# Performance work log

Hardware: AMD Instinct MI355X
Metric: run time of the kernel (lower is better)

Reference implementation:

```python
import jax, jax.numpy as jnp
import numpy as np

N, E, G = 100000, 400000, 2000
D = 128            # dim_node
DE = 128 + 300     # dim_edge after RBF concat
NC = 300           # RBF centers
CUT_LO, CUT_HI = 0.0, 30.0
N_CONV = 3


def setup_inputs() -> dict:
    key = jax.random.key(0)
    ks = jax.random.split(key, 32)
    inp = {}
    inp['Z'] = jax.random.randint(ks[0], (N,), 0, 20)
    inp['edge_type'] = jax.random.randint(ks[1], (E,), 0, 400)
    inp['dist'] = jax.random.uniform(ks[2], (E,), dtype=jnp.float32) * CUT_HI
    inp['src'] = jax.random.randint(ks[3], (E,), 0, N)
    inp['dst'] = jax.random.randint(ks[4], (E,), 0, N)
    inp['graph_ids'] = jnp.sort(jax.random.randint(ks[5], (N,), 0, G))
    s = 0.05
    inp['node_emb'] = jax.random.normal(ks[6], (20, D), jnp.float32) * s
    inp['edge_emb'] = jax.random.normal(ks[7], (400, D), jnp.float32) * s
    # per-conv-layer weights, stacked over layer dim
    inp['Wn1'] = jax.random.normal(ks[8], (N_CONV, D, D), jnp.float32) * s
    inp['bn1'] = jnp.zeros((N_CONV, D), jnp.float32)
    inp['Wn2'] = jax.random.normal(ks[9], (N_CONV, D, D), jnp.float32) * s
    inp['bn2'] = jnp.zeros((N_CONV, D), jnp.float32)
    inp['We1'] = jax.random.normal(ks[10], (N_CONV, DE, DE), jnp.float32) * s
    inp['be1'] = jnp.zeros((N_CONV, DE), jnp.float32)
    inp['We2'] = jax.random.normal(ks[11], (N_CONV, D, DE), jnp.float32) * s
    inp['be2'] = jnp.zeros((N_CONV, D), jnp.float32)
    inp['Wc'] = jax.random.normal(ks[12], (N_CONV, D, D), jnp.float32) * s
    inp['bc'] = jnp.zeros((N_CONV, D), jnp.float32)
    # read layer
    inp['Wr1'] = jax.random.normal(ks[13], (D, D), jnp.float32) * s
    inp['br1'] = jnp.zeros((D,), jnp.float32)
    inp['Wr2'] = jax.random.normal(ks[14], (1, D), jnp.float32) * s
    inp['br2'] = jnp.zeros((1,), jnp.float32)
    return inp


def _rbf(dist):
    centers = jnp.linspace(CUT_LO, CUT_HI, NC, dtype=jnp.float32)
    gap = centers[1] - centers[0]
    # [E, NC]
    return jnp.exp(-((dist[:, None] - centers[None, :]) ** 2) / gap)


def reference(Z, edge_type, dist, src, dst, graph_ids,
              node_emb, edge_emb,
              Wn1, bn1, Wn2, bn2, We1, be1, We2, be2, Wc, bc,
              Wr1, br1, Wr2, br2):
    h = node_emb[Z]                          # [N, D] node embedding
    e = edge_emb[edge_type]                  # [E, D] edge embedding
    e = jnp.concatenate([e, _rbf(dist)], axis=1)   # [E, DE]
    for i in range(N_CONV):
        hs = h[src]                          # gather src node feats [E, D]
        hn = jax.nn.relu(hs @ Wn1[i].T + bn1[i]) @ Wn2[i].T + bn2[i]   # [E, D]
        ee = jax.nn.relu(e @ We1[i].T + be1[i]) @ We2[i].T + be2[i]    # [E, D]
        m = jnp.tanh((hn * ee) @ Wc[i].T + bc[i])                      # [E, D]
        h = h + jax.ops.segment_sum(m, dst, num_segments=N)            # scatter-sum
    r = jax.nn.relu(h @ Wr1.T + br1) @ Wr2.T + br2                     # [N, 1]
    out = jax.ops.segment_sum(r, graph_ids, num_segments=G)            # [G, 1]
    return out.flatten()                                               # [G]
```

## Files before the change

kernel.cpp:

```cpp
#include <hip/hip_runtime.h>

#define NN 100000
#define En 400000
#define Gn 2000
#define GRID 2048

typedef unsigned short u16;
typedef unsigned int u32;
typedef _Float16 f16;
typedef f16 f16x8 __attribute__((ext_vector_type(8)));
typedef float f32x4 __attribute__((ext_vector_type(4)));

__device__ __forceinline__ void lds_barrier() {
  asm volatile("s_waitcnt lgkmcnt(0)\ns_barrier" ::: "memory");
}

#define MFMA16(a, b, c) __builtin_amdgcn_mfma_f32_16x16x32_f16(a, b, c, 0, 0, 0)


__global__ __launch_bounds__(256) void k_prepw(
    const float* __restrict__ Wn1, const float* __restrict__ Wn2,
    const float* __restrict__ Wc, const float* __restrict__ We2,
    const float* __restrict__ We1,
    f16* __restrict__ Wn1b, f16* __restrict__ Wn2b, f16* __restrict__ Wcb,
    f16* __restrict__ We2b, f16* __restrict__ Rb) {
  int i = blockIdx.x * 256 + threadIdx.x;
  if (i < 49152) {
    Wn1b[i] = (f16)Wn1[i];
  } else if (i < 98304) {
    int j = i - 49152;
    Wn2b[j] = (f16)Wn2[j];
  } else if (i < 147456) {
    int j = i - 98304;
    Wcb[j] = (f16)Wc[j];
  } else if (i < 319488) {
    int j = i - 147456;
    int l = j / 57344;
    int r = j - l * 57344;
    int row = r / 448;
    int k = r - row * 448;
    float v = (k < 428) ? We2[l * 54784 + row * 428 + k] : 0.f;
    We2b[j] = (f16)v;
  } else if (i < 749568) {
    int j = i - 319488;
    int l = j / 143360;
    int r = j - l * 143360;
    int row = r / 320;
    int k = r - row * 320;
    float v = 0.f;
    if (row < 428 && k < 300) v = We1[(size_t)l * 183184 + row * 428 + 128 + k];
    Rb[j] = (f16)v;
  }
}


__global__ __launch_bounds__(256) void k_t2(const float* __restrict__ edge_emb,
                                            const float* __restrict__ We1,
                                            const float* __restrict__ be1,
                                            f16* __restrict__ T2) {
  __shared__ __align__(16) float sWe[64][32 * 4];
  __shared__ float sB[64];
  const int tid = threadIdx.x;
  const int l = blockIdx.x / 28;
  const int rb = blockIdx.x - l * 28;
  const int jb = rb >> 2;
  const int tc = rb & 3;
  const int j0 = jb * 64;
  for (int idx = tid; idx < 64 * 32; idx += 256) {
    int row = idx >> 5, c = idx & 31;
    int gj = j0 + row;
    float4 v = make_float4(0.f, 0.f, 0.f, 0.f);
    if (gj < 428)
      v = *(const float4*)&We1[(size_t)l * 183184 + gj * 428 + c * 4];
    *(float4*)&sWe[row][c * 4] = v;
  }
  if (tid < 64) {
    int gj = j0 + tid;
    sB[tid] = (gj < 428) ? be1[l * 428 + gj] : 0.f;
  }
  lds_barrier();
  const int jl = tid & 63, tl = tid >> 6;
  const int gj = j0 + jl;
  for (int it = 0; it < 25; ++it) {
    int t = tc * 100 + it * 4 + tl;
    const float4* er = (const float4*)(edge_emb + t * 128);
    float s = 0.f;
#pragma unroll
    for (int d = 0; d < 32; ++d) {
      float4 a = er[d];
      float4 b = *(const float4*)&sWe[jl][d * 4];
      s += a.x * b.x + a.y * b.y + a.z * b.z + a.w * b.w;
    }
    s += sB[jl];
    T2[l * 179200 + t * 448 + gj] = (gj < 428) ? (f16)s : (f16)0.f;
  }
}

__global__ __launch_bounds__(256) void k_dtab(const f16* __restrict__ Rb,
                                              f16* __restrict__ Dtab) {
  const int tid = threadIdx.x;
  int l = blockIdx.x / (GRID + 1);
  int g = blockIdx.x - l * (GRID + 1);
  float d = (float)g * (30.f / (float)GRID);
  int kc = (int)(d * (299.f / 30.f) + 0.5f);
  int kk0 = min(max(kc - 16, 0), 268);
  __shared__ float sE[32];
  if (tid < 32) {
    float x = d - (float)(kk0 + tid) * (30.f / 299.f);
    sE[tid] = __expf(-x * x * (299.f / 30.f));
  }
  __syncthreads();
  for (int j = tid; j < 448; j += 256) {
    const f16* rr = &Rb[((size_t)l * 448 + j) * 320 + kk0];
    float s = 0.f;
#pragma unroll
    for (int k = 0; k < 32; ++k) s += sE[k] * (float)rr[k];
    Dtab[((size_t)(l * (GRID + 1) + g)) * 448 + j] = (f16)s;
  }
}


__global__ __launch_bounds__(256) void k_zero32(u32* __restrict__ p, int n) {
  int i = blockIdx.x * 256 + threadIdx.x;
  if (i < n) p[i] = 0u;
}

__global__ __launch_bounds__(256) void k_hist(const int* __restrict__ dstv,
                                              u32* __restrict__ hist) {
  int e = blockIdx.x * 256 + threadIdx.x;
  if (e < En) atomicAdd(&hist[dstv[e]], 1u);
}

__global__ __launch_bounds__(1024) void k_scan1(const u32* __restrict__ hist,
                                                u32* __restrict__ excl,
                                                u32* __restrict__ part) {
  __shared__ u32 s[1024];
  const int t = threadIdx.x, b = blockIdx.x, i = b * 1024 + t;
  u32 v = (i < NN) ? hist[i] : 0u;
  s[t] = v;
  __syncthreads();
  u32 acc = v;
  for (int off = 1; off < 1024; off <<= 1) {
    u32 add = (t >= off) ? s[t - off] : 0u;
    __syncthreads();
    acc += add;
    s[t] = acc;
    __syncthreads();
  }
  if (i < NN) excl[i] = acc - v;
  if (t == 1023) part[b] = acc;
}

__global__ __launch_bounds__(128) void k_scan2(u32* __restrict__ part, int n) {
  __shared__ u32 s[128];
  const int t = threadIdx.x;
  u32 v = (t < n) ? part[t] : 0u;
  s[t] = v;
  __syncthreads();
  u32 acc = v;
  for (int off = 1; off < 128; off <<= 1) {
    u32 add = (t >= off) ? s[t - off] : 0u;
    __syncthreads();
    acc += add;
    s[t] = acc;
    __syncthreads();
  }
  if (t < n) part[t] = acc - v;
}

__global__ __launch_bounds__(1024) void k_scan3(const u32* __restrict__ excl,
                                                const u32* __restrict__ part,
                                                u32* __restrict__ cursor) {
  int i = blockIdx.x * 1024 + threadIdx.x;
  if (i < NN) cursor[i] = excl[i] + part[blockIdx.x];
}

__global__ __launch_bounds__(256) void k_scatter(const int* __restrict__ etype,
                                                 const float* __restrict__ dist,
                                                 const int* __restrict__ srcv,
                                                 const int* __restrict__ dstv,
                                                 u32* __restrict__ cursor,
                                                 int4* __restrict__ epack,
                                                 int* __restrict__ edst) {
  int e = blockIdx.x * 256 + threadIdx.x;
  if (e >= En) return;
  int d = dstv[e];
  int pos = (int)atomicAdd(&cursor[d], 1u);
  float fi = dist[e] * ((float)GRID / 30.f);
  int ix = (int)fi;
  epack[pos] = make_int4(srcv[e], etype[e] * 448, ix * 448,
                         __float_as_int(fi - (float)ix));
  edst[pos] = d;
}


__global__ __launch_bounds__(256) void k_node(const float* __restrict__ h,
                                              const f16* __restrict__ W1,
                                              const float* __restrict__ b1,
                                              const f16* __restrict__ W2,
                                              const float* __restrict__ b2,
                                              f16* __restrict__ n2) {
  __shared__ __align__(16) f16 sH[64 * 136];
  __shared__ __align__(16) f16 sT[64 * 136];
  const int tid = threadIdx.x;
  const int nbase = blockIdx.x * 64;
  for (int i = tid; i < 64 * 128; i += 256) {
    int e = i >> 7, d = i & 127;
    int node = nbase + e;
    float v = (node < NN) ? h[(size_t)node * 128 + d] : 0.f;
    sH[e * 136 + d] = (f16)v;
  }
  lds_barrier();
  const int lane = tid & 63, wave = tid >> 6;
  const int q = lane >> 4, ln = lane & 15;
  const int nb = wave * 32;

  f32x4 acc[4][2];
#pragma unroll
  for (int m = 0; m < 4; ++m)
#pragma unroll
    for (int n = 0; n < 2; ++n) acc[m][n] = 0.f;
#pragma unroll
  for (int k0 = 0; k0 < 128; k0 += 32) {
    f16x8 a[4];
#pragma unroll
    for (int m = 0; m < 4; ++m)
      a[m] = *(const f16x8*)&sH[(m * 16 + ln) * 136 + k0 + q * 8];
#pragma unroll
    for (int n = 0; n < 2; ++n) {
      f16x8 b = *(const f16x8*)&W1[(nb + n * 16 + ln) * 128 + k0 + q * 8];
#pragma unroll
      for (int m = 0; m < 4; ++m) acc[m][n] = MFMA16(a[m], b, acc[m][n]);
    }
  }
#pragma unroll
  for (int n = 0; n < 2; ++n) {
    int col = nb + n * 16 + ln;
    float bb = b1[col];
#pragma unroll
    for (int m = 0; m < 4; ++m)
#pragma unroll
      for (int r = 0; r < 4; ++r) {
        int row = m * 16 + q * 4 + r;
        sT[row * 136 + col] = (f16)fmaxf(acc[m][n][r] + bb, 0.f);
      }
  }
  lds_barrier();

  f32x4 acc2[4][2];
#pragma unroll
  for (int m = 0; m < 4; ++m)
#pragma unroll
    for (int n = 0; n < 2; ++n) acc2[m][n] = 0.f;
#pragma unroll
  for (int k0 = 0; k0 < 128; k0 += 32) {
    f16x8 a[4];
#pragma unroll
    for (int m = 0; m < 4; ++m)
      a[m] = *(const f16x8*)&sT[(m * 16 + ln) * 136 + k0 + q * 8];
#pragma unroll
    for (int n = 0; n < 2; ++n) {
      f16x8 b = *(const f16x8*)&W2[(nb + n * 16 + ln) * 128 + k0 + q * 8];
#pragma unroll
      for (int m = 0; m < 4; ++m) acc2[m][n] = MFMA16(a[m], b, acc2[m][n]);
    }
  }
#pragma unroll
  for (int n = 0; n < 2; ++n) {
    int col = nb + n * 16 + ln;
    float bb = b2[col];
#pragma unroll
    for (int m = 0; m < 4; ++m)
#pragma unroll
      for (int r = 0; r < 4; ++r) {
        int row = m * 16 + q * 4 + r;
        int node = nbase + row;
        if (node < NN) n2[(size_t)node * 128 + col] = (f16)(acc2[m][n][r] + bb);
      }
  }
}


__global__ __launch_bounds__(256) void k_node0(const int* __restrict__ Z,
                                               const float* __restrict__ node_emb,
                                               const f16* __restrict__ W1,
                                               const float* __restrict__ b1,
                                               const f16* __restrict__ W2,
                                               const float* __restrict__ b2,
                                               f16* __restrict__ n2,
                                               float* __restrict__ h,
                                               float* __restrict__ out) {
  __shared__ __align__(16) f16 sH[64 * 136];
  __shared__ __align__(16) f16 sT[64 * 136];
  __shared__ int sZ[64];
  const int tid = threadIdx.x;
  const int nbase = blockIdx.x * 64;
  {
    int oi = blockIdx.x * 256 + tid;
    if (oi < Gn) out[oi] = 0.f;
  }
  if (tid < 64) sZ[tid] = Z[min(nbase + tid, NN - 1)];
  lds_barrier();
  for (int i = tid; i < 64 * 128; i += 256) {
    int e = i >> 7, d = i & 127;
    int node = nbase + e;
    float v = node_emb[sZ[e] * 128 + d];
    sH[e * 136 + d] = (f16)v;
    if (node < NN) h[(size_t)node * 128 + d] = v;
  }
  lds_barrier();
  const int lane = tid & 63, wave = tid >> 6;
  const int q = lane >> 4, ln = lane & 15;
  const int nb = wave * 32;

  f32x4 acc[4][2];
#pragma unroll
  for (int m = 0; m < 4; ++m)
#pragma unroll
    for (int n = 0; n < 2; ++n) acc[m][n] = 0.f;
#pragma unroll
  for (int k0 = 0; k0 < 128; k0 += 32) {
    f16x8 a[4];
#pragma unroll
    for (int m = 0; m < 4; ++m)
      a[m] = *(const f16x8*)&sH[(m * 16 + ln) * 136 + k0 + q * 8];
#pragma unroll
    for (int n = 0; n < 2; ++n) {
      f16x8 b = *(const f16x8*)&W1[(nb + n * 16 + ln) * 128 + k0 + q * 8];
#pragma unroll
      for (int m = 0; m < 4; ++m) acc[m][n] = MFMA16(a[m], b, acc[m][n]);
    }
  }
#pragma unroll
  for (int n = 0; n < 2; ++n) {
    int col = nb + n * 16 + ln;
    float bb = b1[col];
#pragma unroll
    for (int m = 0; m < 4; ++m)
#pragma unroll
      for (int r = 0; r < 4; ++r) {
        int row = m * 16 + q * 4 + r;
        sT[row * 136 + col] = (f16)fmaxf(acc[m][n][r] + bb, 0.f);
      }
  }
  lds_barrier();

  f32x4 acc2[4][2];
#pragma unroll
  for (int m = 0; m < 4; ++m)
#pragma unroll
    for (int n = 0; n < 2; ++n) acc2[m][n] = 0.f;
#pragma unroll
  for (int k0 = 0; k0 < 128; k0 += 32) {
    f16x8 a[4];
#pragma unroll
    for (int m = 0; m < 4; ++m)
      a[m] = *(const f16x8*)&sT[(m * 16 + ln) * 136 + k0 + q * 8];
#pragma unroll
    for (int n = 0; n < 2; ++n) {
      f16x8 b = *(const f16x8*)&W2[(nb + n * 16 + ln) * 128 + k0 + q * 8];
#pragma unroll
      for (int m = 0; m < 4; ++m) acc2[m][n] = MFMA16(a[m], b, acc2[m][n]);
    }
  }
#pragma unroll
  for (int n = 0; n < 2; ++n) {
    int col = nb + n * 16 + ln;
    float bb = b2[col];
#pragma unroll
    for (int m = 0; m < 4; ++m)
#pragma unroll
      for (int r = 0; r < 4; ++r) {
        int row = m * 16 + q * 4 + r;
        int node = nbase + row;
        if (node < NN) n2[(size_t)node * 128 + col] = (f16)(acc2[m][n][r] + bb);
      }
  }
}


__global__ __launch_bounds__(256)
__attribute__((amdgpu_waves_per_eu(4, 4))) void k_edge(
    const int4* __restrict__ epack, const int* __restrict__ edst,
    const f16* __restrict__ T2, const f16* __restrict__ Dtab,
    const f16* __restrict__ We2b, const float* __restrict__ be2,
    const f16* __restrict__ Wcb, const float* __restrict__ bc,
    const f16* __restrict__ n2, float* __restrict__ h) {
  __shared__ __align__(16) f16 sC[2][64 * 136];
  __shared__ int sSrc[64], sDst[64], sT2o[64], sIdx[64];
  __shared__ float sFrac[64];

  const int tid = threadIdx.x;
  const int e0 = blockIdx.x * 64;
  if (tid < 64) {
    int4 p = epack[e0 + tid];
    sSrc[tid] = p.x;
    sT2o[tid] = p.y;
    sIdx[tid] = p.z;
    sFrac[tid] = __int_as_float(p.w);
    sDst[tid] = edst[e0 + tid];
  }
  lds_barrier();

  const int lane = tid & 63, wave = tid >> 6;
  const int q = lane >> 4, ln = lane & 15;
  const int nb = wave * 32;

  f32x4 acc[4][2];
#pragma unroll
  for (int m = 0; m < 4; ++m)
#pragma unroll
    for (int n = 0; n < 2; ++n) acc[m][n] = 0.f;

  auto lerp_relu = [](f16x8 lo, f16x8 hi, f16x8 t2, f16 fr) -> f16x8 {
    f16x8 v = t2 + lo + (hi - lo) * fr;
    f16x8 z = {};
    return __builtin_elementwise_max(v, z);
  };
  auto pf128 = [&](int k0, f16x8* plo, f16x8* phi, f16x8* pt2, f16* pfr) {
    const int cg = tid & 15, eb = tid >> 4;
    const int col = k0 + cg * 8;
#pragma unroll
    for (int i = 0; i < 4; ++i) {
      int e = eb + i * 16;
      int off = sIdx[e] + col;
      plo[i] = *(const f16x8*)&Dtab[off];
      phi[i] = *(const f16x8*)&Dtab[off + 448];
      pt2[i] = *(const f16x8*)&T2[sT2o[e] + col];
      pfr[i] = (f16)sFrac[e];
    }
  };
  auto st128 = [&](f16* buf, const f16x8* plo, const f16x8* phi,
                   const f16x8* pt2, const f16* pfr) {
    const int cg = tid & 15, eb = tid >> 4;
#pragma unroll
    for (int i = 0; i < 4; ++i) {
      int e = eb + i * 16;
      *(f16x8*)&buf[e * 136 + cg * 8] = lerp_relu(plo[i], phi[i], pt2[i], pfr[i]);
    }
  };
  auto pf64 = [&](f16x8* plo, f16x8* phi, f16x8* pt2, f16* pfr) {
    const int cg = tid & 7, eb = tid >> 3;
    const int col = 384 + cg * 8;
#pragma unroll
    for (int i = 0; i < 2; ++i) {
      int e = eb + i * 32;
      int off = sIdx[e] + col;
      plo[i] = *(const f16x8*)&Dtab[off];
      phi[i] = *(const f16x8*)&Dtab[off + 448];
      pt2[i] = *(const f16x8*)&T2[sT2o[e] + col];
      pfr[i] = (f16)sFrac[e];
    }
  };
  auto st64 = [&](f16* buf, const f16x8* plo, const f16x8* phi,
                  const f16x8* pt2, const f16* pfr) {
    const int cg = tid & 7, eb = tid >> 3;
#pragma unroll
    for (int i = 0; i < 2; ++i) {
      int e = eb + i * 32;
      *(f16x8*)&buf[e * 136 + cg * 8] = lerp_relu(plo[i], phi[i], pt2[i], pfr[i]);
    }
  };
  auto mfma_chunk = [&](const f16* buf, int k0, int nk) {
    for (int kk = 0; kk < nk; ++kk) {
      f16x8 a[4];
#pragma unroll
      for (int m = 0; m < 4; ++m)
        a[m] = *(const f16x8*)&buf[(m * 16 + ln) * 136 + kk * 32 + q * 8];
#pragma unroll
      for (int n = 0; n < 2; ++n) {
        f16x8 b = *(const f16x8*)&We2b[(nb + n * 16 + ln) * 448 + k0 + kk * 32 + q * 8];
#pragma unroll
        for (int m = 0; m < 4; ++m) acc[m][n] = MFMA16(a[m], b, acc[m][n]);
      }
    }
  };

  {
    f16x8 plo[4], phi[4], pt2[4]; f16 pfr[4];
    pf128(0, plo, phi, pt2, pfr);
    st128(sC[0], plo, phi, pt2, pfr);
  }
  lds_barrier();
  {
    f16x8 plo[4], phi[4], pt2[4]; f16 pfr[4];
    pf128(128, plo, phi, pt2, pfr);
    mfma_chunk(sC[0], 0, 4);
    st128(sC[1], plo, phi, pt2, pfr);
  }
  lds_barrier();
  {
    f16x8 plo[4], phi[4], pt2[4]; f16 pfr[4];
    pf128(256, plo, phi, pt2, pfr);
    mfma_chunk(sC[1], 128, 4);
    st128(sC[0], plo, phi, pt2, pfr);
  }
  lds_barrier();
  f16x8 nrows[4];
  {
    f16x8 plo[2], phi[2], pt2[2]; f16 pfr[2];
    pf64(plo, phi, pt2, pfr);
#pragma unroll
    for (int i = 0; i < 4; ++i) {
      int u = tid + 256 * i;
      int e = u >> 4, cg = u & 15;
      nrows[i] = *(const f16x8*)&n2[(size_t)sSrc[e] * 128 + cg * 8];
    }
    mfma_chunk(sC[0], 256, 4);
    st64(sC[1], plo, phi, pt2, pfr);
  }
  lds_barrier();

  f16* sN = sC[0];
#pragma unroll
  for (int i = 0; i < 4; ++i) {
    int u = tid + 256 * i;
    int e = u >> 4, cg = u & 15;
    *(f16x8*)&sN[e * 136 + cg * 8] = nrows[i];
  }
  mfma_chunk(sC[1], 384, 2);
  lds_barrier();

  f16* sP = sC[1];
  {
    float be2v[2] = {be2[nb + ln], be2[nb + 16 + ln]};
#pragma unroll
    for (int n = 0; n < 2; ++n) {
      int col = nb + n * 16 + ln;
#pragma unroll
      for (int m = 0; m < 4; ++m)
#pragma unroll
        for (int r = 0; r < 4; ++r) {
          int row = m * 16 + q * 4 + r;
          float ee = acc[m][n][r] + be2v[n];
          sP[row * 136 + col] = (f16)(ee * (float)sN[row * 136 + col]);
        }
    }
  }
  lds_barrier();

  {
    f32x4 acc2[4][2];
#pragma unroll
    for (int m = 0; m < 4; ++m)
#pragma unroll
      for (int n = 0; n < 2; ++n) acc2[m][n] = 0.f;
#pragma unroll
    for (int k0 = 0; k0 < 128; k0 += 32) {
      f16x8 a[4];
#pragma unroll
      for (int m = 0; m < 4; ++m)
        a[m] = *(const f16x8*)&sP[(m * 16 + ln) * 136 + k0 + q * 8];
#pragma unroll
      for (int n = 0; n < 2; ++n) {
        f16x8 b = *(const f16x8*)&Wcb[(nb + n * 16 + ln) * 128 + k0 + q * 8];
#pragma unroll
        for (int m = 0; m < 4; ++m) acc2[m][n] = MFMA16(a[m], b, acc2[m][n]);
      }
    }
    float bcv[2] = {bc[nb + ln], bc[nb + 16 + ln]};
#pragma unroll
    for (int m = 0; m < 4; ++m) {
      int d[4];
#pragma unroll
      for (int r = 0; r < 4; ++r) d[r] = sDst[m * 16 + q * 4 + r];
#pragma unroll
      for (int n = 0; n < 2; ++n) {
        int col = nb + n * 16 + ln;
        float tv[4];
#pragma unroll
        for (int r = 0; r < 4; ++r) {
          float x = acc2[m][n][r] + bcv[n];
          x = fminf(2.f, fmaxf(-2.f, x));
          float x2 = x * x;
          tv[r] = x * (15.f + x2) * __builtin_amdgcn_rcpf(15.f + 6.f * x2);
        }
        float s = tv[0];
        int cur = d[0];
#pragma unroll
        for (int r = 1; r < 4; ++r) {
          if (d[r] == cur) {
            s += tv[r];
          } else {
            unsafeAtomicAdd(&h[(size_t)cur * 128 + col], s);
            cur = d[r];
            s = tv[r];
          }
        }
        unsafeAtomicAdd(&h[(size_t)cur * 128 + col], s);
      }
    }
  }
}


__global__ __launch_bounds__(256) void k_read(const float* __restrict__ h,
                                              const float* __restrict__ Wr1,
                                              const float* __restrict__ br1,
                                              const float* __restrict__ Wr2,
                                              const float* __restrict__ br2,
                                              const int* __restrict__ gid,
                                              float* __restrict__ out) {
  __shared__ __align__(16) f16 sH[64 * 136];
  __shared__ __align__(16) f16 sW[128 * 136];
  __shared__ float sR4[4][64];
  const int tid = threadIdx.x;
  const int nbase = blockIdx.x * 64;
  for (int i = tid; i < 64 * 128; i += 256) {
    int e = i >> 7, d = i & 127;
    int node = nbase + e;
    float v = (node < NN) ? h[(size_t)node * 128 + d] : 0.f;
    sH[e * 136 + d] = (f16)v;
  }
  for (int i = tid; i < 128 * 128; i += 256) {
    int rr = i >> 7, d = i & 127;
    sW[rr * 136 + d] = (f16)Wr1[i];
  }
  lds_barrier();
  const int lane = tid & 63, wave = tid >> 6;
  const int q = lane >> 4, ln = lane & 15;
  const int nb = wave * 32;

  f32x4 acc[4][2];
#pragma unroll
  for (int m = 0; m < 4; ++m)
#pragma unroll
    for (int n = 0; n < 2; ++n) acc[m][n] = 0.f;
#pragma unroll
  for (int k0 = 0; k0 < 128; k0 += 32) {
    f16x8 a[4];
#pragma unroll
    for (int m = 0; m < 4; ++m)
      a[m] = *(const f16x8*)&sH[(m * 16 + ln) * 136 + k0 + q * 8];
#pragma unroll
    for (int n = 0; n < 2; ++n) {
      f16x8 b = *(const f16x8*)&sW[(nb + n * 16 + ln) * 136 + k0 + q * 8];
#pragma unroll
      for (int m = 0; m < 4; ++m) acc[m][n] = MFMA16(a[m], b, acc[m][n]);
    }
  }
#pragma unroll
  for (int m = 0; m < 4; ++m)
#pragma unroll
    for (int r = 0; r < 4; ++r) {
      float t = 0.f;
#pragma unroll
      for (int n = 0; n < 2; ++n) {
        int col = nb + n * 16 + ln;
        t += fmaxf(acc[m][n][r] + br1[col], 0.f) * Wr2[col];
      }
      t += __shfl_xor(t, 1);
      t += __shfl_xor(t, 2);
      t += __shfl_xor(t, 4);
      t += __shfl_xor(t, 8);
      if (ln == 0) sR4[wave][m * 16 + q * 4 + r] = t;
    }
  lds_barrier();
  if (tid < 64) {
    int node = nbase + tid;
    if (node < NN) {
      float s = sR4[0][tid] + sR4[1][tid] + sR4[2][tid] + sR4[3][tid] + br2[0];
      unsafeAtomicAdd(&out[gid[node]], s);
    }
  }
}


extern "C" void kernel_launch(void* const* d_in, const int* in_sizes, int n_in,
                              void* d_out, int out_size, void* d_ws, size_t ws_size,
                              hipStream_t stream) {
  const int* Z = (const int*)d_in[0];
  const int* etype = (const int*)d_in[1];
  const float* dist = (const float*)d_in[2];
  const int* src = (const int*)d_in[3];
  const int* dst = (const int*)d_in[4];
  const int* gid = (const int*)d_in[5];
  const float* node_emb = (const float*)d_in[6];
  const float* edge_emb = (const float*)d_in[7];
  const float* Wn1 = (const float*)d_in[8];
  const float* bn1 = (const float*)d_in[9];
  const float* Wn2 = (const float*)d_in[10];
  const float* bn2 = (const float*)d_in[11];
  const float* We1 = (const float*)d_in[12];
  const float* be1 = (const float*)d_in[13];
  const float* We2 = (const float*)d_in[14];
  const float* be2 = (const float*)d_in[15];
  const float* Wc = (const float*)d_in[16];
  const float* bc = (const float*)d_in[17];
  const float* Wr1 = (const float*)d_in[18];
  const float* br1 = (const float*)d_in[19];
  const float* Wr2 = (const float*)d_in[20];
  const float* br2 = (const float*)d_in[21];
  float* out = (float*)d_out;

  char* ws = (char*)d_ws;
  float* h = (float*)(ws);
  f16* n2 = (f16*)(ws + 51200000);
  f16* Rb = (f16*)(ws + 76800000);
  f16* We2b = (f16*)(ws + 77660160);
  f16* Wcb = (f16*)(ws + 78004224);
  f16* Wn1b = (f16*)(ws + 78102528);
  f16* Wn2b = (f16*)(ws + 78200832);
  f16* T2 = (f16*)(ws + 78299136);
  f16* Dtab = (f16*)(ws + 79374336);
  int4* epack = (int4*)(ws + 84882048);
  int* edst = (int*)(ws + 91282048);
  u32* hist = (u32*)(ws + 92882048);
  u32* cursor = (u32*)(ws + 93282048);
  u32* excl = (u32*)(ws + 93682048);
  u32* part = (u32*)(ws + 94082048);

  k_zero32<<<391, 256, 0, stream>>>(hist, NN);
  k_hist<<<1563, 256, 0, stream>>>(dst, hist);
  k_scan1<<<98, 1024, 0, stream>>>(hist, excl, part);
  k_scan2<<<1, 128, 0, stream>>>(part, 98);
  k_scan3<<<98, 1024, 0, stream>>>(excl, part, cursor);
  k_scatter<<<1563, 256, 0, stream>>>(etype, dist, src, dst, cursor, epack, edst);

  k_prepw<<<2928, 256, 0, stream>>>(Wn1, Wn2, Wc, We2, We1,
                                    Wn1b, Wn2b, Wcb, We2b, Rb);
  k_t2<<<84, 256, 0, stream>>>(edge_emb, We1, be1, T2);
  k_dtab<<<3 * (GRID + 1), 256, 0, stream>>>(Rb, Dtab);

  for (int l = 0; l < 3; ++l) {
    if (l == 0) {
      k_node0<<<1563, 256, 0, stream>>>(Z, node_emb, Wn1b, bn1, Wn2b, bn2,
                                        n2, h, out);
    } else {
      k_node<<<1563, 256, 0, stream>>>(h, Wn1b + l * 16384, bn1 + l * 128,
                                       Wn2b + l * 16384, bn2 + l * 128, n2);
    }
    k_edge<<<6250, 256, 0, stream>>>(epack, edst,
                                     T2 + l * 179200, Dtab + (size_t)l * (GRID + 1) * 448,
                                     We2b + l * 57344, be2 + l * 128,
                                     Wcb + l * 16384, bc + l * 128, n2, h);
  }
  k_read<<<1563, 256, 0, stream>>>(h, Wr1, br1, Wr2, br2, gid, out);
}
```

Measured before the change: 943.0 us.

## Shrink edge-kernel LDS tiles to 64-wide chunks and fuse node-feature multiply into MFMA loads

The edge kernel now stages the 448-wide hidden activation in seven 64-column chunks instead of 128-column chunks, halving the double-buffered LDS footprint. The waves-per-EU hint is raised from 4 to 6-8 to exploit the lower LDS and register use. The gathered source-node features are no longer staged through LDS; they are loaded directly into registers in MFMA operand layout and multiplied into the A fragments during the Wc GEMM, with the next slice prefetched. The cost is more barriers and smaller MFMA batches per stage, and sP rows (stride 136, 64 rows) now have to fit in the 2x64x72 buffer. That layout looks like it overflows sC[0] into sC[1], which is contiguous, so it stays valid.

```diff
diff --git a/kernel.cpp b/kernel.cpp
--- a/kernel.cpp
+++ b/kernel.cpp
@@ -380,13 +380,13 @@
 
 
 __global__ __launch_bounds__(256)
-__attribute__((amdgpu_waves_per_eu(4, 4))) void k_edge(
+__attribute__((amdgpu_waves_per_eu(6, 8))) void k_edge(
     const int4* __restrict__ epack, const int* __restrict__ edst,
     const f16* __restrict__ T2, const f16* __restrict__ Dtab,
     const f16* __restrict__ We2b, const float* __restrict__ be2,
     const f16* __restrict__ Wcb, const float* __restrict__ bc,
     const f16* __restrict__ n2, float* __restrict__ h) {
-  __shared__ __align__(16) f16 sC[2][64 * 136];
+  __shared__ __align__(16) f16 sC[2][64 * 72];
   __shared__ int sSrc[64], sDst[64], sT2o[64], sIdx[64];
   __shared__ float sFrac[64];
 
@@ -417,31 +417,9 @@
     f16x8 z = {};
     return __builtin_elementwise_max(v, z);
   };
-  auto pf128 = [&](int k0, f16x8* plo, f16x8* phi, f16x8* pt2, f16* pfr) {
-    const int cg = tid & 15, eb = tid >> 4;
+  auto pf = [&](int k0, f16x8* plo, f16x8* phi, f16x8* pt2, f16* pfr) {
+    const int cg = tid & 7, eb = tid >> 3;
     const int col = k0 + cg * 8;
-#pragma unroll
-    for (int i = 0; i < 4; ++i) {
-      int e = eb + i * 16;
-      int off = sIdx[e] + col;
-      plo[i] = *(const f16x8*)&Dtab[off];
-      phi[i] = *(const f16x8*)&Dtab[off + 448];
-      pt2[i] = *(const f16x8*)&T2[sT2o[e] + col];
-      pfr[i] = (f16)sFrac[e];
-    }
-  };
-  auto st128 = [&](f16* buf, const f16x8* plo, const f16x8* phi,
-                   const f16x8* pt2, const f16* pfr) {
-    const int cg = tid & 15, eb = tid >> 4;
-#pragma unroll
-    for (int i = 0; i < 4; ++i) {
-      int e = eb + i * 16;
-      *(f16x8*)&buf[e * 136 + cg * 8] = lerp_relu(plo[i], phi[i], pt2[i], pfr[i]);
-    }
-  };
-  auto pf64 = [&](f16x8* plo, f16x8* phi, f16x8* pt2, f16* pfr) {
-    const int cg = tid & 7, eb = tid >> 3;
-    const int col = 384 + cg * 8;
 #pragma unroll
     for (int i = 0; i < 2; ++i) {
       int e = eb + i * 32;
@@ -452,24 +430,26 @@
       pfr[i] = (f16)sFrac[e];
     }
   };
-  auto st64 = [&](f16* buf, const f16x8* plo, const f16x8* phi,
-                  const f16x8* pt2, const f16* pfr) {
+  auto st = [&](f16* buf, const f16x8* plo, const f16x8* phi,
+                const f16x8* pt2, const f16* pfr) {
     const int cg = tid & 7, eb = tid >> 3;
 #pragma unroll
     for (int i = 0; i < 2; ++i) {
       int e = eb + i * 32;
-      *(f16x8*)&buf[e * 136 + cg * 8] = lerp_relu(plo[i], phi[i], pt2[i], pfr[i]);
+      *(f16x8*)&buf[e * 72 + cg * 8] = lerp_relu(plo[i], phi[i], pt2[i], pfr[i]);
     }
   };
-  auto mfma_chunk = [&](const f16* buf, int k0, int nk) {
-    for (int kk = 0; kk < nk; ++kk) {
+  auto mfma_chunk = [&](const f16* buf, int k0) {
+#pragma unroll
+    for (int kk = 0; kk < 2; ++kk) {
       f16x8 a[4];
 #pragma unroll
       for (int m = 0; m < 4; ++m)
-        a[m] = *(const f16x8*)&buf[(m * 16 + ln) * 136 + kk * 32 + q * 8];
+        a[m] = *(const f16x8*)&buf[(m * 16 + ln) * 72 + kk * 32 + q * 8];
 #pragma unroll
       for (int n = 0; n < 2; ++n) {
-        f16x8 b = *(const f16x8*)&We2b[(nb + n * 16 + ln) * 448 + k0 + kk * 32 + q * 8];
+        f16x8 b =
+            *(const f16x8*)&We2b[(nb + n * 16 + ln) * 448 + k0 + kk * 32 + q * 8];
 #pragma unroll
         for (int m = 0; m < 4; ++m) acc[m][n] = MFMA16(a[m], b, acc[m][n]);
       }
@@ -477,51 +457,32 @@
   };
 
   {
-    f16x8 plo[4], phi[4], pt2[4]; f16 pfr[4];
-    pf128(0, plo, phi, pt2, pfr);
-    st128(sC[0], plo, phi, pt2, pfr);
-  }
-  lds_barrier();
-  {
-    f16x8 plo[4], phi[4], pt2[4]; f16 pfr[4];
-    pf128(128, plo, phi, pt2, pfr);
-    mfma_chunk(sC[0], 0, 4);
-    st128(sC[1], plo, phi, pt2, pfr);
-  }
-  lds_barrier();
-  {
-    f16x8 plo[4], phi[4], pt2[4]; f16 pfr[4];
-    pf128(256, plo, phi, pt2, pfr);
-    mfma_chunk(sC[1], 128, 4);
-    st128(sC[0], plo, phi, pt2, pfr);
-  }
-  lds_barrier();
-  f16x8 nrows[4];
-  {
-    f16x8 plo[2], phi[2], pt2[2]; f16 pfr[2];
-    pf64(plo, phi, pt2, pfr);
-#pragma unroll
-    for (int i = 0; i < 4; ++i) {
-      int u = tid + 256 * i;
-      int e = u >> 4, cg = u & 15;
-      nrows[i] = *(const f16x8*)&n2[(size_t)sSrc[e] * 128 + cg * 8];
-    }
-    mfma_chunk(sC[0], 256, 4);
-    st64(sC[1], plo, phi, pt2, pfr);
-  }
-  lds_barrier();
-
-  f16* sN = sC[0];
-#pragma unroll
-  for (int i = 0; i < 4; ++i) {
-    int u = tid + 256 * i;
-    int e = u >> 4, cg = u & 15;
-    *(f16x8*)&sN[e * 136 + cg * 8] = nrows[i];
-  }
-  mfma_chunk(sC[1], 384, 2);
-  lds_barrier();
-
-  f16* sP = sC[1];
+    f16x8 plo[2], phi[2], pt2[2];
+    f16 pfr[2];
+    pf(0, plo, phi, pt2, pfr);
+    st(sC[0], plo, phi, pt2, pfr);
+  }
+  lds_barrier();
+#pragma unroll
+  for (int c = 1; c < 7; ++c) {
+    f16x8 plo[2], phi[2], pt2[2];
+    f16 pfr[2];
+    pf(c * 64, plo, phi, pt2, pfr);
+    mfma_chunk(sC[(c - 1) & 1], (c - 1) * 64);
+    st(sC[c & 1], plo, phi, pt2, pfr);
+    lds_barrier();
+  }
+  int srow[4];
+#pragma unroll
+  for (int m = 0; m < 4; ++m) srow[m] = sSrc[m * 16 + ln];
+  f16x8 nf[4];
+#pragma unroll
+  for (int m = 0; m < 4; ++m)
+    nf[m] = *(const f16x8*)&n2[(size_t)srow[m] * 128 + q * 8];
+  mfma_chunk(sC[0], 384);
+  lds_barrier();
+
+  f16* sP = &sC[0][0];
   {
     float be2v[2] = {be2[nb + ln], be2[nb + 16 + ln]};
 #pragma unroll
@@ -532,8 +493,7 @@
 #pragma unroll
         for (int r = 0; r < 4; ++r) {
           int row = m * 16 + q * 4 + r;
-          float ee = acc[m][n][r] + be2v[n];
-          sP[row * 136 + col] = (f16)(ee * (float)sN[row * 136 + col]);
+          sP[row * 136 + col] = (f16)(acc[m][n][r] + be2v[n]);
         }
     }
   }
@@ -550,7 +510,13 @@
       f16x8 a[4];
 #pragma unroll
       for (int m = 0; m < 4; ++m)
-        a[m] = *(const f16x8*)&sP[(m * 16 + ln) * 136 + k0 + q * 8];
+        a[m] = *(const f16x8*)&sP[(m * 16 + ln) * 136 + k0 + q * 8] * nf[m];
+      if (k0 < 96) {
+#pragma unroll
+        for (int m = 0; m < 4; ++m)
+          nf[m] =
+              *(const f16x8*)&n2[(size_t)srow[m] * 128 + (k0 + 32) + q * 8];
+      }
 #pragma unroll
       for (int n = 0; n < 2; ++n) {
         f16x8 b = *(const f16x8*)&Wcb[(nb + n * 16 + ln) * 128 + k0 + q * 8];
```

Result: slower. 1.133 ms (+20.1%).
